# Kernel optimization log

Measured on AMD Instinct MI355X. Metric: run time of the kernel, lower is better.

Reference implementation:

```python
import jax, jax.numpy as jnp
import numpy as np

K = 10      # neighbors; conv width math 10 -> 3 -> 1
EPS = 1e-5  # InstanceNorm2d default eps (affine=False)
NEG = 0.2   # leaky relu slope


def _instnorm(x):
    m = x.mean(axis=(2, 3), keepdims=True)
    v = x.var(axis=(2, 3), keepdims=True)  # biased var, as in torch instance_norm
    return (x - m) * jax.lax.rsqrt(v + EPS)


def _conv13(x, w, b, s):
    y = jax.lax.conv_general_dilated(x, w, (1, s), 'VALID',
                                     dimension_numbers=('NCHW', 'OIHW', 'NCHW'))
    return y + b[None, :, None, None]


def _block(x, wA, bA, wB, bB):
    # Sequential(conv(1,3,stride(1,3)), IN, ReLU, conv(1,3), IN, ReLU)
    y = jax.nn.relu(_instnorm(_conv13(x, wA, bA, 3)))
    return jax.nn.relu(_instnorm(_conv13(y, wB, bB, 1)))


def _knn_idx(coords, k):
    # coords [B,2,N] -> k nearest neighbor indices [B,N,k] (self excluded)
    pts = coords.transpose(0, 2, 1)
    sq = (pts ** 2).sum(-1)
    dist = sq[:, :, None] + sq[:, None, :] - 2.0 * jnp.einsum('bnc,bmc->bnm', pts, pts)
    dist = jnp.clip(dist, 1e-12)
    _, idx = jax.lax.top_k(-dist, k + 1)  # smallest distances, sorted
    return idx[:, :, 1:]


def _gather_nb(x, idx):
    # x [B,C,N], idx [B,N,k] -> [B,C,N,k]
    return jax.vmap(lambda f, i: f[:, i])(x, idx)


def _graph_feat(feats, idx):
    nb = _gather_nb(feats, idx)
    ctr = jnp.broadcast_to(feats[..., None], nb.shape)
    return jnp.concatenate([ctr, nb - ctr], axis=1)  # [B,2C,N,k]


def _cos_angle(coords, idx):
    nei = _gather_nb(coords, idx)          # [B,2,N,k]
    ctr = coords[..., None]                # [B,2,N,1]
    dot = (ctr * nei).sum(axis=1, keepdims=True)
    na = jnp.sqrt((ctr ** 2).sum(axis=1, keepdims=True))
    nb = jnp.sqrt((nei ** 2).sum(axis=1, keepdims=True))
    return dot / (na * nb)                 # [B,1,N,k]


def _c1(w, x):
    # 1x1 conv, no bias
    return jnp.einsum('oi,bihw->bohw', w, x)


def _forward(coords, features, W1, W2, W3, W3o, a1wA, a1bA, a1wB, a1bB,
             a2wA, a2bA, a2wB, a2bB, angwA, angbA, angwB, angbB):
    B, C, N = features.shape
    lrelu = lambda x: jax.nn.leaky_relu(x, NEG)
    x0 = features[..., None]
    # KNN depends only on coords: all three torch graph builds give identical indices
    idx = _knn_idx(coords, K)
    x1_old = _graph_feat(features, idx)                         # [B,2C,N,K]
    x1 = _block(x1_old, a1wA, a1bA, a1wB, a1bB)                 # [B,C,N,1]
    # angle_enc1 is shared and idx identical -> f_ang1 == f_ang2
    f_ang = _block(_cos_angle(coords, idx), angwA, angbA, angwB, angbB)
    x2 = _block(_graph_feat(x1[..., 0], idx), a2wA, a2bA, a2wB, a2bB)
    x3 = jnp.concatenate([x0, x1 + f_ang, x2 + f_ang], axis=1)  # [B,3C,N,1]
    x3 = lrelu(_instnorm(_c1(W3, x3))).reshape(B, -1, N)
    x1o = lrelu(_instnorm(_c1(W1, x1_old))).max(axis=-1, keepdims=True)   # [B,C,N,1]
    x2o = lrelu(_instnorm(_c1(W2, _graph_feat(x1o[..., 0], idx)))).max(axis=-1, keepdims=True)
    x3o = jnp.concatenate([x0, x1o, x2o], axis=1)               # [B,4C,N,1]
    x3o = lrelu(_instnorm(_c1(W3o, x3o))).reshape(B, -1, N)
    return x3 + x3o


def setup_inputs():
    key = jax.random.key(0)
    ks = jax.random.split(key, 20)
    B, C, N = 4, 128, 4096
    r = lambda i, shp, sc=1.0: jax.random.normal(ks[i], shp, jnp.float32) * sc
    s = 0.05
    return {
        'coords': r(0, (B, 2, N)),
        'features': r(1, (B, C, N)),
        'W1': r(2, (C, 2 * C), s),
        'W2': r(3, (2 * C, 2 * C), s),
        'W3': r(4, (C, 3 * C), s),
        'W3o': r(5, (C, 4 * C), s),
        'a1wA': r(6, (C, 2 * C, 1, 3), s), 'a1bA': r(7, (C,), s),
        'a1wB': r(8, (C, C, 1, 3), s), 'a1bB': r(9, (C,), s),
        'a2wA': r(10, (C, 2 * C, 1, 3), s), 'a2bA': r(11, (C,), s),
        'a2wB': r(12, (C, C, 1, 3), s), 'a2bB': r(13, (C,), s),
        'angwA': r(14, (C, 1, 1, 3), s), 'angbA': r(15, (C,), s),
        'angwB': r(16, (C, C, 1, 3), s), 'angbB': r(17, (C,), s),
    }


def reference(coords, features, W1, W2, W3, W3o, a1wA, a1bA, a1wB, a1bB,
              a2wA, a2bA, a2wB, a2bB, angwA, angbA, angwB, angbB):
    return _forward(coords, features, W1, W2, W3, W3o, a1wA, a1bA, a1wB, a1bB,
                    a2wA, a2bA, a2wB, a2bB, angwA, angbA, angwB, angbB)
```

## Files before the change

kernel.cpp:

```cpp
#include <hip/hip_runtime.h>
#include <hip/hip_bf16.h>

typedef unsigned long long ull;

#define BN 4
#define CH 128
#define NP 4096
#define KNB 10
#define EPSI 1e-5f
#define GM_PTS 16
#define CA_PTS 16

#define FMA4(A, W, F) do { (A).x += (W).x*(F); (A).y += (W).y*(F); \
                           (A).z += (W).z*(F); (A).w += (W).w*(F); } while(0)

__device__ __forceinline__ ull shfl_xor_u64(ull v, int mask) {
    unsigned lo = (unsigned)(v & 0xFFFFFFFFu);
    unsigned hi = (unsigned)(v >> 32);
    lo = __shfl_xor(lo, mask);
    hi = __shfl_xor(hi, mask);
    return ((ull)hi << 32) | lo;
}

__device__ __forceinline__ int clampj(int j) { return ((unsigned)j < (unsigned)NP) ? j : 0; }

__device__ __forceinline__ unsigned short f2bf(float f) {
    unsigned u = __float_as_uint(f);
    unsigned r = u + 0x7FFFu + ((u >> 16) & 1u);
    return (unsigned short)(r >> 16);
}
__device__ __forceinline__ float bf2f(unsigned short h) {
    return __uint_as_float(((unsigned)h) << 16);
}
__device__ __forceinline__ float4 bfload4(const unsigned short* p) {
    ushort4 h = *(const ushort4*)p;
    float4 r; r.x = bf2f(h.x); r.y = bf2f(h.y); r.z = bf2f(h.z); r.w = bf2f(h.w);
    return r;
}
__device__ __forceinline__ ushort4 bf4(float4 x) {
    ushort4 h; h.x = f2bf(x.x); h.y = f2bf(x.y); h.z = f2bf(x.z); h.w = f2bf(x.w);
    return h;
}

__device__ __forceinline__ void d_packA(const float* w, float* WT, int i) {
    int co = i % CH, ci = (i / CH) % CH, s = i / (CH * CH);
    float val;
    if (s == 0) {
        val = 0.f;
        for (int dk = 0; dk < 3; dk++)
            val += w[(co * 256 + ci) * 3 + dk] - w[(co * 256 + 128 + ci) * 3 + dk];
    } else {
        val = w[(co * 256 + 128 + ci) * 3 + (s - 1)];
    }
    WT[i] = val;
}
__device__ __forceinline__ void d_packB(const float* w, float* WT, int i) {
    int co = i % CH, ci = (i / CH) % CH, dk = i / (CH * CH);
    WT[i] = w[(co * CH + ci) * 3 + dk];
}
__device__ __forceinline__ void d_packUV(const float* w, float* Wu, float* Wn, int Cout, int i) {
    int co = i % Cout, ci = i / Cout;
    float a = w[co * 256 + ci], bb = w[co * 256 + 128 + ci];
    Wu[i] = a - bb; Wn[i] = bb;
}
__device__ __forceinline__ void d_packP(const float* w, float* WT, int Cin, int Cout, int i) {
    int co = i % Cout, ci = i / Cout;
    WT[i] = w[co * Cin + ci];
}

__global__ void pack_all(const float* __restrict__ a1wA, const float* __restrict__ a2wA,
                         const float* __restrict__ a1wB, const float* __restrict__ a2wB,
                         const float* __restrict__ angwB, const float* __restrict__ W1,
                         const float* __restrict__ W2, const float* __restrict__ W3,
                         const float* __restrict__ W3o, const float* __restrict__ angwA,
                         float* __restrict__ WA1T, float* __restrict__ WA2T,
                         float* __restrict__ WB1T, float* __restrict__ WB2T,
                         float* __restrict__ WBAT,
                         float* __restrict__ W1U, float* __restrict__ W1N,
                         float* __restrict__ W2U, float* __restrict__ W2N,
                         float* __restrict__ W3T, float* __restrict__ W3OT,
                         float* __restrict__ WANGA) {
    int i = blockIdx.x * 256 + threadIdx.x;
    const int sA = 4 * CH * CH;
    const int sB = 3 * CH * CH;
    if (i < sA) { d_packA(a1wA, WA1T, i); return; } i -= sA;
    if (i < sA) { d_packA(a2wA, WA2T, i); return; } i -= sA;
    if (i < sB) { d_packB(a1wB, WB1T, i); return; } i -= sB;
    if (i < sB) { d_packB(a2wB, WB2T, i); return; } i -= sB;
    if (i < sB) { d_packB(angwB, WBAT, i); return; } i -= sB;
    if (i < CH * CH) { d_packUV(W1, W1U, W1N, CH, i); return; } i -= CH * CH;
    if (i < CH * 256) { d_packUV(W2, W2U, W2N, 256, i); return; } i -= CH * 256;
    if (i < 384 * CH) { d_packP(W3, W3T, 384, CH, i); return; } i -= 384 * CH;
    if (i < 512 * CH) { d_packP(W3o, W3OT, 512, CH, i); return; } i -= 512 * CH;
    if (i < 3 * CH) { d_packP(angwA, WANGA, 3, CH, i); return; }
}

__global__ void ftrans_kernel(const float* __restrict__ feats, float* __restrict__ F) {
    int i = blockIdx.x * 256 + threadIdx.x;
    if (i >= BN * CH * NP) return;
    int n = i % NP, c = (i / NP) % CH, b = i / (NP * CH);
    F[(b * NP + n) * CH + c] = feats[i];
}

__global__ void knn_kernel(const float* __restrict__ coords, int* __restrict__ IDX) {
    int gw = blockIdx.x * 4 + (threadIdx.x >> 6);
    int b = gw / NP;
    int n = gw % NP;
    int lane = threadIdx.x & 63;
    float xn = coords[(b * 2 + 0) * NP + n];
    float yn = coords[(b * 2 + 1) * NP + n];
    float sn = __fadd_rn(__fmul_rn(xn, xn), __fmul_rn(yn, yn));
    ull a[11];
    #pragma unroll
    for (int q = 0; q < 11; q++) a[q] = 0xFFFFFFFFFFFFFFFFULL;
    for (int m = lane; m < NP; m += 64) {
        float xm = coords[(b * 2 + 0) * NP + m];
        float ym = coords[(b * 2 + 1) * NP + m];
        float sm = __fadd_rn(__fmul_rn(xm, xm), __fmul_rn(ym, ym));
        float dot = __fmaf_rn(yn, ym, __fmul_rn(xn, xm));
        float d = __fsub_rn(__fadd_rn(sn, sm), __fmul_rn(2.0f, dot));
        d = fmaxf(d, 1e-12f);
        ull key = ((ull)__float_as_uint(d) << 32) | (unsigned)m;
        if (key < a[10]) {
            a[10] = key;
            #pragma unroll
            for (int q = 10; q > 0; --q)
                if (a[q] < a[q - 1]) { ull t = a[q]; a[q] = a[q - 1]; a[q - 1] = t; }
        }
    }
    for (int r = 0; r < 11; ++r) {
        ull k = a[0];
        ull mk = k;
        #pragma unroll
        for (int off = 1; off < 64; off <<= 1) {
            ull o = shfl_xor_u64(mk, off);
            mk = (o < mk) ? o : mk;
        }
        if (k == mk) {
            #pragma unroll
            for (int q = 0; q < 10; ++q) a[q] = a[q + 1];
            a[10] = 0xFFFFFFFFFFFFFFFFULL;
        }
        if (lane == 0 && r > 0) IDX[(b * NP + n) * KNB + (r - 1)] = (int)(mk & 0xFFFFFFFFu);
    }
}

__global__ void cosangle_kernel(const float* __restrict__ coords, const int* __restrict__ IDX,
                                float* __restrict__ COSA) {
    int i = blockIdx.x * 256 + threadIdx.x;
    if (i >= BN * NP * KNB) return;
    int n = (i / KNB) % NP, b = i / (KNB * NP);
    int j = clampj(IDX[i]);
    float xc = coords[(b * 2 + 0) * NP + n], yc = coords[(b * 2 + 1) * NP + n];
    float xm = coords[(b * 2 + 0) * NP + j], ym = coords[(b * 2 + 1) * NP + j];
    float dot = xc * xm + yc * ym;
    float na = sqrtf(xc * xc + yc * yc);
    float nb2 = sqrtf(xm * xm + ym * ym);
    COSA[i] = dot / fmaxf(na * nb2, 1e-30f);
}

__global__ __launch_bounds__(256) void convA_kernel(const float* __restrict__ Fin,
                             const int* __restrict__ IDX,
                             const float* __restrict__ WT, float* __restrict__ YA,
                             float* __restrict__ PART,
                             const float* __restrict__ STATS, int slot) {
    __shared__ __align__(16) float ctr[CA_PTS][CH];
    __shared__ __align__(16) unsigned short nbh[CA_PTS][9][CH];
    __shared__ int jidx[CA_PTS * 9];
    int b = blockIdx.x / (NP / CA_PTS);
    int chunk = blockIdx.x % (NP / CA_PTS);
    int n0 = chunk * CA_PTS;
    int cog = threadIdx.x & 31;
    int pg  = threadIdx.x >> 5;
    const float* SB = (slot >= 0) ? &STATS[((size_t)(slot * BN + b) * 256) * 2] : nullptr;
    if (threadIdx.x < CA_PTS * 9) {
        int n = threadIdx.x / 9, kk = threadIdx.x % 9;
        jidx[threadIdx.x] = clampj(IDX[(b * NP + n0 + n) * KNB + kk]);
    }
    __syncthreads();
    for (int v4 = threadIdx.x; v4 < CA_PTS * 32; v4 += 256) {
        int n = v4 >> 5, c4 = v4 & 31;
        float4 x = *(const float4*)&Fin[(size_t)(b * NP + n0 + n) * CH + c4 * 4];
        if (SB) {
            float4 s0 = *(const float4*)&SB[c4 * 8];
            float4 s1 = *(const float4*)&SB[c4 * 8 + 4];
            x.x = fmaxf((x.x - s0.x) * s0.y, 0.f);
            x.y = fmaxf((x.y - s0.z) * s0.w, 0.f);
            x.z = fmaxf((x.z - s1.x) * s1.y, 0.f);
            x.w = fmaxf((x.w - s1.z) * s1.w, 0.f);
        }
        *(float4*)&ctr[n][c4 * 4] = x;
    }
    for (int v4 = threadIdx.x; v4 < CA_PTS * 9 * 32; v4 += 256) {
        int n = v4 / 288, rem = v4 % 288, kk = rem >> 5, c4 = rem & 31;
        float4 x = *(const float4*)&Fin[(size_t)(b * NP + jidx[n * 9 + kk]) * CH + c4 * 4];
        if (SB) {
            float4 s0 = *(const float4*)&SB[c4 * 8];
            float4 s1 = *(const float4*)&SB[c4 * 8 + 4];
            x.x = fmaxf((x.x - s0.x) * s0.y, 0.f);
            x.y = fmaxf((x.y - s0.z) * s0.w, 0.f);
            x.z = fmaxf((x.z - s1.x) * s1.y, 0.f);
            x.w = fmaxf((x.w - s1.z) * s1.w, 0.f);
        }
        *(ushort4*)&nbh[n][kk][c4 * 4] = bf4(x);
    }
    __syncthreads();
    const float4* W4 = (const float4*)WT;
    const int p0 = pg * 2, p1 = pg * 2 + 1;
    float4 cacc0, cacc1;
    cacc0.x = cacc0.y = cacc0.z = cacc0.w = 0.f;
    cacc1 = cacc0;
    for (int ci = 0; ci < CH; ci += 4) {
        float4 xa = *(const float4*)&ctr[p0][ci];
        float4 xb = *(const float4*)&ctr[p1][ci];
        #pragma unroll
        for (int u = 0; u < 4; ++u) {
            float4 w = W4[(ci + u) * 32 + cog];
            float fa = ((const float*)&xa)[u];
            float fb = ((const float*)&xb)[u];
            FMA4(cacc0, w, fa); FMA4(cacc1, w, fb);
        }
    }
    float4 t00 = cacc0, t01 = cacc0, t02 = cacc0;
    float4 t10 = cacc1, t11 = cacc1, t12 = cacc1;
    for (int dk = 0; dk < 3; ++dk) {
        const float4* Wd = W4 + (size_t)(1 + dk) * (CH * 32);
        const unsigned short* a00 = &nbh[p0][0 * 3 + dk][0];
        const unsigned short* a01 = &nbh[p0][1 * 3 + dk][0];
        const unsigned short* a02 = &nbh[p0][2 * 3 + dk][0];
        const unsigned short* a10 = &nbh[p1][0 * 3 + dk][0];
        const unsigned short* a11 = &nbh[p1][1 * 3 + dk][0];
        const unsigned short* a12 = &nbh[p1][2 * 3 + dk][0];
        for (int ci = 0; ci < CH; ci += 4) {
            float4 x00 = bfload4(&a00[ci]);
            float4 x01 = bfload4(&a01[ci]);
            float4 x02 = bfload4(&a02[ci]);
            float4 x10 = bfload4(&a10[ci]);
            float4 x11 = bfload4(&a11[ci]);
            float4 x12 = bfload4(&a12[ci]);
            #pragma unroll
            for (int u = 0; u < 4; ++u) {
                float4 w = Wd[(ci + u) * 32 + cog];
                FMA4(t00, w, ((const float*)&x00)[u]);
                FMA4(t01, w, ((const float*)&x01)[u]);
                FMA4(t02, w, ((const float*)&x02)[u]);
                FMA4(t10, w, ((const float*)&x10)[u]);
                FMA4(t11, w, ((const float*)&x11)[u]);
                FMA4(t12, w, ((const float*)&x12)[u]);
            }
        }
    }
    {
        size_t base0 = ((size_t)(b * NP + n0 + p0) * 3) * CH + cog * 4;
        *(float4*)&YA[base0 + 0 * CH] = t00;
        *(float4*)&YA[base0 + 1 * CH] = t01;
        *(float4*)&YA[base0 + 2 * CH] = t02;
        size_t base1 = ((size_t)(b * NP + n0 + p1) * 3) * CH + cog * 4;
        *(float4*)&YA[base1 + 0 * CH] = t10;
        *(float4*)&YA[base1 + 1 * CH] = t11;
        *(float4*)&YA[base1 + 2 * CH] = t12;
    }
    float s4[4], q4[4];
    s4[0] = t00.x + t01.x + t02.x + t10.x + t11.x + t12.x;
    s4[1] = t00.y + t01.y + t02.y + t10.y + t11.y + t12.y;
    s4[2] = t00.z + t01.z + t02.z + t10.z + t11.z + t12.z;
    s4[3] = t00.w + t01.w + t02.w + t10.w + t11.w + t12.w;
    q4[0] = t00.x*t00.x + t01.x*t01.x + t02.x*t02.x + t10.x*t10.x + t11.x*t11.x + t12.x*t12.x;
    q4[1] = t00.y*t00.y + t01.y*t01.y + t02.y*t02.y + t10.y*t10.y + t11.y*t11.y + t12.y*t12.y;
    q4[2] = t00.z*t00.z + t01.z*t01.z + t02.z*t02.z + t10.z*t10.z + t11.z*t11.z + t12.z*t12.z;
    q4[3] = t00.w*t00.w + t01.w*t01.w + t02.w*t02.w + t10.w*t10.w + t11.w*t11.w + t12.w*t12.w;
    __syncthreads();
    float* red = (float*)&nbh[0][0][0];
    #pragma unroll
    for (int j = 0; j < 4; ++j) {
        red[((pg * 32 + cog) * 4 + j) * 2 + 0] = s4[j];
        red[((pg * 32 + cog) * 4 + j) * 2 + 1] = q4[j];
    }
    __syncthreads();
    if (threadIdx.x < CH) {
        int c = threadIdx.x;
        float ss = 0.f, qq = 0.f;
        #pragma unroll
        for (int g = 0; g < 8; ++g) {
            ss += red[((g * 32 + (c >> 2)) * 4 + (c & 3)) * 2 + 0];
            qq += red[((g * 32 + (c >> 2)) * 4 + (c & 3)) * 2 + 1];
        }
        PART[((size_t)(b * (NP / CA_PTS) + chunk) * 256 + c) * 2 + 0] = ss;
        PART[((size_t)(b * (NP / CA_PTS) + chunk) * 256 + c) * 2 + 1] = qq;
    }
}

__global__ void angA_kernel(const float* __restrict__ COSA, const float* __restrict__ WT,
                            float* __restrict__ YA, float* __restrict__ PART) {
    __shared__ float ca[32][10];
    int b = blockIdx.x / (NP / 32);
    int chunk = blockIdx.x % (NP / 32);
    int n0 = chunk * 32;
    int co = threadIdx.x;
    for (int v = threadIdx.x; v < 320; v += 128) {
        int nn = v / 10, kk = v % 10;
        ca[nn][kk] = COSA[(b * NP + n0 + nn) * KNB + kk];
    }
    float w0 = WT[co], w1 = WT[CH + co], w2 = WT[2 * CH + co];
    __syncthreads();
    float sum = 0.f, sq = 0.f;
    for (int nn = 0; nn < 32; nn++) {
        #pragma unroll
        for (int t = 0; t < 3; t++) {
            float v = w0 * ca[nn][3 * t] + w1 * ca[nn][3 * t + 1] + w2 * ca[nn][3 * t + 2];
            YA[((b * NP + n0 + nn) * 3 + t) * CH + co] = v;
            sum += v; sq += v * v;
        }
    }
    PART[((b * (NP / 32) + chunk) * 256 + co) * 2 + 0] = sum;
    PART[((b * (NP / 32) + chunk) * 256 + co) * 2 + 1] = sq;
}

template <int CIN, int NCOG>
__device__ __forceinline__ void gemm_16pt(const float* lds, const float* __restrict__ WT,
                                          int cog, int pg, float4 acc[4]) {
    const float4* W4 = (const float4*)WT;
    const float* xb = lds + pg * 4 * CIN;
    for (int ci = 0; ci < CIN; ci += 4) {
        float4 x0 = *(const float4*)&xb[0 * CIN + ci];
        float4 x1 = *(const float4*)&xb[1 * CIN + ci];
        float4 x2 = *(const float4*)&xb[2 * CIN + ci];
        float4 x3 = *(const float4*)&xb[3 * CIN + ci];
        #pragma unroll
        for (int u = 0; u < 4; ++u) {
            float4 w = W4[(ci + u) * NCOG + cog];
            float f0 = ((const float*)&x0)[u];
            float f1 = ((const float*)&x1)[u];
            float f2 = ((const float*)&x2)[u];
            float f3 = ((const float*)&x3)[u];
            FMA4(acc[0], w, f0); FMA4(acc[1], w, f1);
            FMA4(acc[2], w, f2); FMA4(acc[3], w, f3);
        }
    }
}

template <int NCOG>
__device__ __forceinline__ void reduce_stats(const float* s4, const float* q4,
                                             float* red, float* __restrict__ PART,
                                             int b, int chunk, int nchunks,
                                             int pg, int cog) {
    constexpr int COUT = NCOG * 4;
    __syncthreads();
    #pragma unroll
    for (int j = 0; j < 4; ++j) {
        red[((pg * NCOG + cog) * 4 + j) * 2 + 0] = s4[j];
        red[((pg * NCOG + cog) * 4 + j) * 2 + 1] = q4[j];
    }
    __syncthreads();
    int c = threadIdx.x;
    if (c < COUT) {
        float ss = 0.f, qq = 0.f;
        #pragma unroll
        for (int g = 0; g < 4; ++g) {
            ss += red[((g * NCOG + (c >> 2)) * 4 + (c & 3)) * 2 + 0];
            qq += red[((g * NCOG + (c >> 2)) * 4 + (c & 3)) * 2 + 1];
        }
        PART[((size_t)(b * nchunks + chunk) * 256 + c) * 2 + 0] = ss;
        PART[((size_t)(b * nchunks + chunk) * 256 + c) * 2 + 1] = qq;
    }
}

template <int NCOG>
__device__ __forceinline__ void out16(const float4 acc[4], float* __restrict__ OUT,
                                      int b, int n0, int pg, int cog,
                                      float s4[4], float q4[4]) {
    constexpr int COUT = NCOG * 4;
    #pragma unroll
    for (int p = 0; p < 4; ++p) {
        *(float4*)&OUT[(size_t)(b * NP + n0 + pg * 4 + p) * COUT + cog * 4] = acc[p];
        s4[0] += acc[p].x; s4[1] += acc[p].y; s4[2] += acc[p].z; s4[3] += acc[p].w;
        q4[0] += acc[p].x * acc[p].x; q4[1] += acc[p].y * acc[p].y;
        q4[2] += acc[p].z * acc[p].z; q4[3] += acc[p].w * acc[p].w;
    }
}

template <int CIN, int NCOG>
__global__ void pixel_gemm_t(const float* __restrict__ IN_, const float* __restrict__ WT,
                             float* __restrict__ OUT, const float* __restrict__ STATS,
                             int slot, int act, float* __restrict__ PART) {
    constexpr int COUT = NCOG * 4;
    constexpr int BD = 4 * NCOG;
    __shared__ __align__(16) float ldsin[16 * CIN];
    int b = blockIdx.x / (NP / 16);
    int chunk = blockIdx.x % (NP / 16);
    int n0 = chunk * 16;
    int cog = threadIdx.x & (NCOG - 1);
    int pg = threadIdx.x / NCOG;
    constexpr int nv4 = 16 * CIN / 4;
    if (slot >= 0) {
        int cbase = (4 * threadIdx.x) & 127;
        const float* st = &STATS[((slot * BN + b) * 256 + cbase) * 2];
        float m0 = st[0], r0 = st[1], m1 = st[2], r1 = st[3];
        float m2 = st[4], r2 = st[5], m3 = st[6], r3 = st[7];
        for (int v4 = threadIdx.x; v4 < nv4; v4 += BD) {
            float4 x = *(const float4*)&IN_[(size_t)(b * NP + n0) * CIN + 4 * v4];
            float v0 = (x.x - m0) * r0, v1 = (x.y - m1) * r1;
            float v2 = (x.z - m2) * r2, v3 = (x.w - m3) * r3;
            if (act) {
                x.x = (v0 >= 0.f) ? v0 : 0.2f * v0;
                x.y = (v1 >= 0.f) ? v1 : 0.2f * v1;
                x.z = (v2 >= 0.f) ? v2 : 0.2f * v2;
                x.w = (v3 >= 0.f) ? v3 : 0.2f * v3;
            } else {
                x.x = fmaxf(v0, 0.f); x.y = fmaxf(v1, 0.f);
                x.z = fmaxf(v2, 0.f); x.w = fmaxf(v3, 0.f);
            }
            *(float4*)&ldsin[4 * v4] = x;
        }
    } else {
        for (int v4 = threadIdx.x; v4 < nv4; v4 += BD)
            *(float4*)&ldsin[4 * v4] =
                *(const float4*)&IN_[(size_t)(b * NP + n0) * CIN + 4 * v4];
    }
    __syncthreads();
    float4 acc[4];
    #pragma unroll
    for (int p = 0; p < 4; ++p) acc[p].x = acc[p].y = acc[p].z = acc[p].w = 0.f;
    gemm_16pt<CIN, NCOG>(ldsin, WT, cog, pg, acc);
    float s4[4] = {0,0,0,0}, q4[4] = {0,0,0,0};
    out16<NCOG>(acc, OUT, b, n0, pg, cog, s4, q4);
    if (PART)
        reduce_stats<NCOG>(s4, q4, ldsin, PART, b, chunk, NP / 16, pg, cog);
}

__global__ void stats_final(const float* __restrict__ PART, float* __restrict__ STATS,
                            int S, int Cc, int slot, int nch) {
    __shared__ float ssum[256], ssq[256];
    int bc = blockIdx.x;
    int b = bc / Cc, c = bc % Cc;
    float sum = 0.f, sq = 0.f;
    for (int ch = threadIdx.x; ch < nch; ch += 256) {
        sum += PART[((b * nch + ch) * 256 + c) * 2 + 0];
        sq  += PART[((b * nch + ch) * 256 + c) * 2 + 1];
    }
    ssum[threadIdx.x] = sum; ssq[threadIdx.x] = sq;
    __syncthreads();
    for (int s = 128; s > 0; s >>= 1) {
        if (threadIdx.x < s) {
            ssum[threadIdx.x] += ssum[threadIdx.x + s];
            ssq[threadIdx.x]  += ssq[threadIdx.x + s];
        }
        __syncthreads();
    }
    if (threadIdx.x == 0) {
        float mean = ssum[0] / (float)S;
        float var = fmaxf(ssq[0] / (float)S - mean * mean, 0.f);
        STATS[((slot * BN + b) * 256 + c) * 2 + 0] = mean;
        STATS[((slot * BN + b) * 256 + c) * 2 + 1] = rsqrtf(var + EPSI);
    }
}

template <int NCOG>
__global__ void gathermax_t(const float* __restrict__ X, const float* __restrict__ Wu,
                            const float* __restrict__ V, const int* __restrict__ IDX,
                            float* __restrict__ M, float* __restrict__ PART,
                            const float* __restrict__ STATS, int slot) {
    constexpr int COUT = NCOG * 4;
    __shared__ __align__(16) float rows[GM_PTS * CH];
    int b = blockIdx.x / (NP / GM_PTS);
    int chunk = blockIdx.x % (NP / GM_PTS);
    int n0 = chunk * GM_PTS;
    int cog = threadIdx.x & (NCOG - 1);
    int pg = threadIdx.x / NCOG;
    if (slot >= 0) {
        int c0 = (4 * threadIdx.x) & 127;
        const float* st = &STATS[((slot * BN + b) * 256 + c0) * 2];
        float m0 = st[0], r0 = st[1], m1 = st[2], r1 = st[3];
        float m2 = st[4], r2 = st[5], m3 = st[6], r3 = st[7];
        for (int v4 = threadIdx.x; v4 < GM_PTS * CH / 4; v4 += COUT) {
            float4 x = *(const float4*)&X[(size_t)(b * NP + n0) * CH + v4 * 4];
            float v0 = (x.x - m0) * r0, v1 = (x.y - m1) * r1;
            float v2 = (x.z - m2) * r2, v3 = (x.w - m3) * r3;
            x.x = (v0 >= 0.f) ? v0 : 0.2f * v0;
            x.y = (v1 >= 0.f) ? v1 : 0.2f * v1;
            x.z = (v2 >= 0.f) ? v2 : 0.2f * v2;
            x.w = (v3 >= 0.f) ? v3 : 0.2f * v3;
            *(float4*)&rows[v4 * 4] = x;
        }
    } else {
        for (int v4 = threadIdx.x; v4 < GM_PTS * CH / 4; v4 += COUT)
            *(float4*)&rows[v4 * 4] = *(const float4*)&X[(size_t)(b * NP + n0) * CH + v4 * 4];
    }
    __syncthreads();
    float4 acc[4];
    #pragma unroll
    for (int p = 0; p < 4; ++p) acc[p].x = acc[p].y = acc[p].z = acc[p].w = 0.f;
    gemm_16pt<CH, NCOG>(rows, Wu, cog, pg, acc);
    float s4[4] = {0,0,0,0}, q4[4] = {0,0,0,0};
    #pragma unroll
    for (int p = 0; p < 4; ++p) {
        int nn = n0 + pg * 4 + p;
        float4 u = acc[p];
        float4 best; best.x = best.y = best.z = best.w = -3.4e38f;
        for (int k = 0; k < KNB; ++k) {
            int j = clampj(IDX[(b * NP + nn) * KNB + k]);
            float4 vv = *(const float4*)&V[(size_t)(b * NP + j) * COUT + cog * 4];
            vv.x += u.x; vv.y += u.y; vv.z += u.z; vv.w += u.w;
            s4[0] += vv.x; s4[1] += vv.y; s4[2] += vv.z; s4[3] += vv.w;
            q4[0] += vv.x * vv.x; q4[1] += vv.y * vv.y;
            q4[2] += vv.z * vv.z; q4[3] += vv.w * vv.w;
            best.x = fmaxf(best.x, vv.x); best.y = fmaxf(best.y, vv.y);
            best.z = fmaxf(best.z, vv.z); best.w = fmaxf(best.w, vv.w);
        }
        *(float4*)&M[(size_t)(b * NP + nn) * COUT + cog * 4] = best;
    }
    __syncthreads();
    reduce_stats<NCOG>(s4, q4, rows, PART, b, chunk, NP / GM_PTS, pg, cog);
}

__global__ void head3_kernel(const float* __restrict__ F, const float* __restrict__ X1,
                             const float* __restrict__ X2, const float* __restrict__ FANG,
                             const float* __restrict__ WT, float* __restrict__ Y3,
                             float* __restrict__ PART, const float* __restrict__ STATS) {
    __shared__ __align__(16) float lds[16 * 384];
    int b = blockIdx.x / (NP / 16);
    int chunk = blockIdx.x % (NP / 16);
    int n0 = chunk * 16;
    int cog = threadIdx.x & 31;
    int pg = threadIdx.x >> 5;
    const float* S1 = &STATS[((size_t)(1 * BN + b) * 256) * 2];
    const float* S5 = &STATS[((size_t)(5 * BN + b) * 256) * 2];
    const float* S3 = &STATS[((size_t)(3 * BN + b) * 256) * 2];
    for (int v4 = threadIdx.x; v4 < 16 * 96; v4 += 128) {
        int nn = v4 / 96, q4 = v4 % 96;
        int part = q4 >> 5, c4 = q4 & 31;
        size_t base = (size_t)(b * NP + n0 + nn) * CH + c4 * 4;
        float4 val;
        if (part == 0) val = *(const float4*)&F[base];
        else {
            const float* src = (part == 1) ? X1 : X2;
            const float* SX = (part == 1) ? S1 : S5;
            float4 xx = *(const float4*)&src[base];
            float4 aa = *(const float4*)&FANG[base];
            float4 sx0 = *(const float4*)&SX[c4 * 8];
            float4 sx1 = *(const float4*)&SX[c4 * 8 + 4];
            float4 sa0 = *(const float4*)&S3[c4 * 8];
            float4 sa1 = *(const float4*)&S3[c4 * 8 + 4];
            val.x = fmaxf((xx.x - sx0.x) * sx0.y, 0.f) + fmaxf((aa.x - sa0.x) * sa0.y, 0.f);
            val.y = fmaxf((xx.y - sx0.z) * sx0.w, 0.f) + fmaxf((aa.y - sa0.z) * sa0.w, 0.f);
            val.z = fmaxf((xx.z - sx1.x) * sx1.y, 0.f) + fmaxf((aa.z - sa1.x) * sa1.y, 0.f);
            val.w = fmaxf((xx.w - sx1.z) * sx1.w, 0.f) + fmaxf((aa.w - sa1.z) * sa1.w, 0.f);
        }
        *(float4*)&lds[v4 * 4] = val;
    }
    __syncthreads();
    float4 acc[4];
    #pragma unroll
    for (int p = 0; p < 4; ++p) acc[p].x = acc[p].y = acc[p].z = acc[p].w = 0.f;
    gemm_16pt<384, 32>(lds, WT, cog, pg, acc);
    float s4[4] = {0,0,0,0}, q4[4] = {0,0,0,0};
    out16<32>(acc, Y3, b, n0, pg, cog, s4, q4);
    reduce_stats<32>(s4, q4, lds, PART, b, chunk, NP / 16, pg, cog);
}

__global__ void head3o_kernel(const float* __restrict__ F, const float* __restrict__ X1O,
                              const float* __restrict__ X2O, const float* __restrict__ WT,
                              float* __restrict__ Y3O, float* __restrict__ PART,
                              const float* __restrict__ STATS) {
    __shared__ __align__(16) float lds[16 * 512];
    int b = blockIdx.x / (NP / 16);
    int chunk = blockIdx.x % (NP / 16);
    int n0 = chunk * 16;
    int cog = threadIdx.x & 31;
    int pg = threadIdx.x >> 5;
    const float* S6 = &STATS[((size_t)(6 * BN + b) * 256) * 2];
    const float* S7 = &STATS[((size_t)(7 * BN + b) * 256) * 2];
    for (int v4 = threadIdx.x; v4 < 16 * 128; v4 += 128) {
        int nn = v4 >> 7, q4 = v4 & 127;
        float4 val;
        if (q4 < 32) {
            val = *(const float4*)&F[(size_t)(b * NP + n0 + nn) * CH + q4 * 4];
        } else if (q4 < 64) {
            int c4 = q4 - 32;
            float4 x = *(const float4*)&X1O[(size_t)(b * NP + n0 + nn) * CH + c4 * 4];
            float4 s0 = *(const float4*)&S6[c4 * 8];
            float4 s1 = *(const float4*)&S6[c4 * 8 + 4];
            float v0 = (x.x - s0.x) * s0.y, v1 = (x.y - s0.z) * s0.w;
            float v2 = (x.z - s1.x) * s1.y, v3 = (x.w - s1.z) * s1.w;
            val.x = (v0 >= 0.f) ? v0 : 0.2f * v0;
            val.y = (v1 >= 0.f) ? v1 : 0.2f * v1;
            val.z = (v2 >= 0.f) ? v2 : 0.2f * v2;
            val.w = (v3 >= 0.f) ? v3 : 0.2f * v3;
        } else {
            int c4 = q4 - 64;
            float4 x = *(const float4*)&X2O[(size_t)(b * NP + n0 + nn) * 256 + c4 * 4];
            float4 s0 = *(const float4*)&S7[c4 * 8];
            float4 s1 = *(const float4*)&S7[c4 * 8 + 4];
            float v0 = (x.x - s0.x) * s0.y, v1 = (x.y - s0.z) * s0.w;
            float v2 = (x.z - s1.x) * s1.y, v3 = (x.w - s1.z) * s1.w;
            val.x = (v0 >= 0.f) ? v0 : 0.2f * v0;
            val.y = (v1 >= 0.f) ? v1 : 0.2f * v1;
            val.z = (v2 >= 0.f) ? v2 : 0.2f * v2;
            val.w = (v3 >= 0.f) ? v3 : 0.2f * v3;
        }
        *(float4*)&lds[v4 * 4] = val;
    }
    __syncthreads();
    float4 acc[4];
    #pragma unroll
    for (int p = 0; p < 4; ++p) acc[p].x = acc[p].y = acc[p].z = acc[p].w = 0.f;
    gemm_16pt<512, 32>(lds, WT, cog, pg, acc);
    float s4[4] = {0,0,0,0}, q4[4] = {0,0,0,0};
    out16<32>(acc, Y3O, b, n0, pg, cog, s4, q4);
    reduce_stats<32>(s4, q4, lds, PART, b, chunk, NP / 16, pg, cog);
}

__global__ void final_kernel(const float* __restrict__ Y3, const float* __restrict__ Y3O,
                             const float* __restrict__ STATS, float* __restrict__ out) {
    __shared__ float T[64][129];
    int b = blockIdx.x / (NP / 64);
    int n0 = (blockIdx.x % (NP / 64)) * 64;
    int co = threadIdx.x;
    float m3 = STATS[((8 * BN + b) * 256 + co) * 2 + 0];
    float r3 = STATS[((8 * BN + b) * 256 + co) * 2 + 1];
    float m3o = STATS[((9 * BN + b) * 256 + co) * 2 + 0];
    float r3o = STATS[((9 * BN + b) * 256 + co) * 2 + 1];
    for (int j = 0; j < 64; j++) {
        size_t idx = (size_t)(b * NP + n0 + j) * CH + co;
        float v3 = (Y3[idx] - m3) * r3;
        v3 = (v3 >= 0.f) ? v3 : 0.2f * v3;
        float v3o = (Y3O[idx] - m3o) * r3o;
        v3o = (v3o >= 0.f) ? v3o : 0.2f * v3o;
        T[j][co] = v3 + v3o;
    }
    __syncthreads();
    for (int rr = 0; rr < 64; rr++) {
        int r = rr * 2 + (threadIdx.x >> 6);
        int j = threadIdx.x & 63;
        out[(size_t)(b * CH + r) * NP + n0 + j] = T[j][r];
    }
}

extern "C" void kernel_launch(void* const* d_in, const int* in_sizes, int n_in,
                              void* d_out, int out_size, void* d_ws, size_t ws_size,
                              hipStream_t stream) {
    const float* coords   = (const float*)d_in[0];
    const float* features = (const float*)d_in[1];
    const float* W1   = (const float*)d_in[2];
    const float* W2   = (const float*)d_in[3];
    const float* W3   = (const float*)d_in[4];
    const float* W3o  = (const float*)d_in[5];
    const float* a1wA = (const float*)d_in[6];
    const float* a1wB = (const float*)d_in[8];
    const float* a2wA = (const float*)d_in[10];
    const float* a2wB = (const float*)d_in[12];
    const float* angwA = (const float*)d_in[14];
    const float* angwB = (const float*)d_in[16];
    float* out = (float*)d_out;
    float* ws = (float*)d_ws;
    (void)ws_size; (void)in_sizes; (void)n_in; (void)out_size;

    size_t off = 0;
    float* WA1T  = ws + off; off += 4 * CH * CH;
    float* WA2T  = ws + off; off += 4 * CH * CH;
    float* WB1T  = ws + off; off += 3 * CH * CH;
    float* WB2T  = ws + off; off += 3 * CH * CH;
    float* WBAT  = ws + off; off += 3 * CH * CH;
    float* WANGA = ws + off; off += 512;
    float* W1U   = ws + off; off += CH * CH;
    float* W1N   = ws + off; off += CH * CH;
    float* W2U   = ws + off; off += CH * 256;
    float* W2N   = ws + off; off += CH * 256;
    float* W3T   = ws + off; off += 384 * CH;
    float* W3OT  = ws + off; off += 512 * CH;
    int*   IDX   = (int*)(ws + off); off += (size_t)BN * NP * KNB;
    float* COSA  = ws + off; off += (size_t)BN * NP * KNB;
    float* PART  = ws + off; off += (size_t)BN * 1024 * 256 * 2;
    float* STATS = ws + off; off += 10 * BN * 256 * 2;
    const size_t UNIT = (size_t)BN * NP * CH;
    float* POOL  = ws + off; off += 7 * UNIT;

    float* F    = POOL + 0 * UNIT;
    float* YA   = POOL + 1 * UNIT;
    float* X1   = POOL + 4 * UNIT;
    float* FANG = POOL + 5 * UNIT;
    float* X2   = POOL + 6 * UNIT;
    float* Y3   = POOL + 1 * UNIT;
    float* V1   = POOL + 2 * UNIT;
    float* M1   = POOL + 6 * UNIT;
    float* V2   = POOL + 4 * UNIT;
    float* M2   = POOL + 2 * UNIT;
    float* Y3O  = POOL + 4 * UNIT;

    pack_all<<<1730, 256, 0, stream>>>(a1wA, a2wA, a1wB, a2wB, angwB, W1, W2, W3, W3o, angwA,
                                       WA1T, WA2T, WB1T, WB2T, WBAT,
                                       W1U, W1N, W2U, W2N, W3T, W3OT, WANGA);

    ftrans_kernel<<<(BN * CH * NP + 255) / 256, 256, 0, stream>>>(features, F);
    knn_kernel<<<BN * NP / 4, 256, 0, stream>>>(coords, IDX);
    cosangle_kernel<<<(BN * NP * KNB + 255) / 256, 256, 0, stream>>>(coords, IDX, COSA);

    auto sfin = [&](int S, int Cc, int slot, int nch) {
        stats_final<<<BN * Cc, 256, 0, stream>>>(PART, STATS, S, Cc, slot, nch);
    };

    convA_kernel<<<BN * (NP / CA_PTS), 256, 0, stream>>>(F, IDX, WA1T, YA, PART, STATS, -1);
    sfin(3 * NP, CH, 0, NP / CA_PTS);
    pixel_gemm_t<384, 32><<<BN * (NP / 16), 128, 0, stream>>>(YA, WB1T, X1, STATS, 0, 0, PART);
    sfin(NP, CH, 1, NP / 16);

    angA_kernel<<<BN * (NP / 32), 128, 0, stream>>>(COSA, WANGA, YA, PART);
    sfin(3 * NP, CH, 2, NP / 32);
    pixel_gemm_t<384, 32><<<BN * (NP / 16), 128, 0, stream>>>(YA, WBAT, FANG, STATS, 2, 0, PART);
    sfin(NP, CH, 3, NP / 16);

    convA_kernel<<<BN * (NP / CA_PTS), 256, 0, stream>>>(X1, IDX, WA2T, YA, PART, STATS, 1);
    sfin(3 * NP, CH, 4, NP / CA_PTS);
    pixel_gemm_t<384, 32><<<BN * (NP / 16), 128, 0, stream>>>(YA, WB2T, X2, STATS, 4, 0, PART);
    sfin(NP, CH, 5, NP / 16);

    head3_kernel<<<BN * (NP / 16), 128, 0, stream>>>(F, X1, X2, FANG, W3T, Y3, PART, STATS);
    sfin(NP, CH, 8, NP / 16);

    pixel_gemm_t<128, 32><<<BN * (NP / 16), 128, 0, stream>>>(F, W1N, V1, STATS, -1, 0, nullptr);
    gathermax_t<32><<<BN * (NP / GM_PTS), 128, 0, stream>>>(F, W1U, V1, IDX, M1, PART, STATS, -1);
    sfin(NP * KNB, CH, 6, NP / GM_PTS);

    pixel_gemm_t<128, 64><<<BN * (NP / 16), 256, 0, stream>>>(M1, W2N, V2, STATS, 6, 1, nullptr);
    gathermax_t<64><<<BN * (NP / GM_PTS), 256, 0, stream>>>(M1, W2U, V2, IDX, M2, PART, STATS, 6);
    sfin(NP * KNB, 256, 7, NP / GM_PTS);

    head3o_kernel<<<BN * (NP / 16), 128, 0, stream>>>(F, M1, M2, W3OT, Y3O, PART, STATS);
    sfin(NP, CH, 9, NP / 16);
    final_kernel<<<BN * (NP / 64), 128, 0, stream>>>(Y3, Y3O, STATS, out);
}
```

Measured before the change: 840.8 us.

## Fuse instance-norm stats finalization into producer kernels via atomics and last-block

```diff
diff --git a/kernel.cpp b/kernel.cpp
--- a/kernel.cpp
+++ b/kernel.cpp
@@ -40,6 +40,35 @@
 __device__ __forceinline__ ushort4 bf4(float4 x) {
     ushort4 h; h.x = f2bf(x.x); h.y = f2bf(x.y); h.z = f2bf(x.z); h.w = f2bf(x.w);
     return h;
+}
+
+__device__ __forceinline__ void stats_commit(float* __restrict__ SACC,
+                                             unsigned* __restrict__ CNT,
+                                             float* __restrict__ STATS,
+                                             int oslot, int b, int c, int valid,
+                                             float ss, float qq, int nblk, float Sdiv) {
+    __shared__ int isLast;
+    if (valid) {
+        atomicAdd(&SACC[((size_t)oslot * (BN * 256) + b * 256 + c) * 2 + 0], ss);
+        atomicAdd(&SACC[((size_t)oslot * (BN * 256) + b * 256 + c) * 2 + 1], qq);
+    }
+    __syncthreads();
+    if (threadIdx.x == 0) {
+        __threadfence();
+        unsigned old = atomicAdd(&CNT[oslot], 1u);
+        isLast = (old == (unsigned)(nblk - 1)) ? 1 : 0;
+    }
+    __syncthreads();
+    if (isLast) {
+        for (int i = threadIdx.x; i < BN * 256; i += blockDim.x) {
+            float sum = atomicAdd(&SACC[((size_t)oslot * (BN * 256) + i) * 2 + 0], 0.f);
+            float sq  = atomicAdd(&SACC[((size_t)oslot * (BN * 256) + i) * 2 + 1], 0.f);
+            float mean = sum / Sdiv;
+            float var = fmaxf(sq / Sdiv - mean * mean, 0.f);
+            STATS[((size_t)oslot * (BN * 256) + i) * 2 + 0] = mean;
+            STATS[((size_t)oslot * (BN * 256) + i) * 2 + 1] = rsqrtf(var + EPSI);
+        }
+    }
 }
 
 __device__ __forceinline__ void d_packA(const float* w, float* WT, int i) {
@@ -79,8 +108,12 @@
                          float* __restrict__ W1U, float* __restrict__ W1N,
                          float* __restrict__ W2U, float* __restrict__ W2N,
                          float* __restrict__ W3T, float* __restrict__ W3OT,
-                         float* __restrict__ WANGA) {
-    int i = blockIdx.x * 256 + threadIdx.x;
+                         float* __restrict__ WANGA,
+                         float* __restrict__ SACC, unsigned* __restrict__ CNT) {
+    int iz = blockIdx.x * 256 + threadIdx.x;
+    if (iz < 10 * BN * 256 * 2) SACC[iz] = 0.f;
+    if (iz < 10) CNT[iz] = 0u;
+    int i = iz;
     const int sA = 4 * CH * CH;
     const int sB = 3 * CH * CH;
     if (i < sA) { d_packA(a1wA, WA1T, i); return; } i -= sA;
@@ -162,8 +195,9 @@
 __global__ __launch_bounds__(256) void convA_kernel(const float* __restrict__ Fin,
                              const int* __restrict__ IDX,
                              const float* __restrict__ WT, float* __restrict__ YA,
-                             float* __restrict__ PART,
-                             const float* __restrict__ STATS, int slot) {
+                             const float* __restrict__ STATS_IN, int slot,
+                             float* __restrict__ SACC, unsigned* __restrict__ CNT,
+                             float* __restrict__ STATS, int oslot) {
     __shared__ __align__(16) float ctr[CA_PTS][CH];
     __shared__ __align__(16) unsigned short nbh[CA_PTS][9][CH];
     __shared__ int jidx[CA_PTS * 9];
@@ -172,7 +206,7 @@
     int n0 = chunk * CA_PTS;
     int cog = threadIdx.x & 31;
     int pg  = threadIdx.x >> 5;
-    const float* SB = (slot >= 0) ? &STATS[((size_t)(slot * BN + b) * 256) * 2] : nullptr;
+    const float* SB = (slot >= 0) ? &STATS_IN[((size_t)(slot * BN + b) * 256) * 2] : nullptr;
     if (threadIdx.x < CA_PTS * 9) {
         int n = threadIdx.x / 9, kk = threadIdx.x % 9;
         jidx[threadIdx.x] = clampj(IDX[(b * NP + n0 + n) * KNB + kk]);
@@ -277,21 +311,24 @@
         red[((pg * 32 + cog) * 4 + j) * 2 + 1] = q4[j];
     }
     __syncthreads();
-    if (threadIdx.x < CH) {
-        int c = threadIdx.x;
-        float ss = 0.f, qq = 0.f;
+    float ss = 0.f, qq = 0.f;
+    int c = threadIdx.x;
+    int valid = (c < CH);
+    if (valid) {
         #pragma unroll
         for (int g = 0; g < 8; ++g) {
             ss += red[((g * 32 + (c >> 2)) * 4 + (c & 3)) * 2 + 0];
             qq += red[((g * 32 + (c >> 2)) * 4 + (c & 3)) * 2 + 1];
         }
-        PART[((size_t)(b * (NP / CA_PTS) + chunk) * 256 + c) * 2 + 0] = ss;
-        PART[((size_t)(b * (NP / CA_PTS) + chunk) * 256 + c) * 2 + 1] = qq;
-    }
+    }
+    stats_commit(SACC, CNT, STATS, oslot, b, c, valid, ss, qq,
+                 BN * (NP / CA_PTS), 3.0f * NP);
 }
 
 __global__ void angA_kernel(const float* __restrict__ COSA, const float* __restrict__ WT,
-                            float* __restrict__ YA, float* __restrict__ PART) {
+                            float* __restrict__ YA,
+                            float* __restrict__ SACC, unsigned* __restrict__ CNT,
+                            float* __restrict__ STATS) {
     __shared__ float ca[32][10];
     int b = blockIdx.x / (NP / 32);
     int chunk = blockIdx.x % (NP / 32);
@@ -312,8 +349,7 @@
             sum += v; sq += v * v;
         }
     }
-    PART[((b * (NP / 32) + chunk) * 256 + co) * 2 + 0] = sum;
-    PART[((b * (NP / 32) + chunk) * 256 + co) * 2 + 1] = sq;
+    stats_commit(SACC, CNT, STATS, 2, b, co, 1, sum, sq, BN * (NP / 32), 3.0f * NP);
 }
 
 template <int CIN, int NCOG>
@@ -340,10 +376,13 @@
 }
 
 template <int NCOG>
-__device__ __forceinline__ void reduce_stats(const float* s4, const float* q4,
-                                             float* red, float* __restrict__ PART,
-                                             int b, int chunk, int nchunks,
-                                             int pg, int cog) {
+__device__ __forceinline__ void reduce_commit(const float* s4, const float* q4,
+                                              float* red,
+                                              float* __restrict__ SACC,
+                                              unsigned* __restrict__ CNT,
+                                              float* __restrict__ STATS,
+                                              int oslot, int b, int nblk, float Sdiv,
+                                              int pg, int cog) {
     constexpr int COUT = NCOG * 4;
     __syncthreads();
     #pragma unroll
@@ -353,16 +392,16 @@
     }
     __syncthreads();
     int c = threadIdx.x;
-    if (c < COUT) {
-        float ss = 0.f, qq = 0.f;
+    float ss = 0.f, qq = 0.f;
+    int valid = (c < COUT);
+    if (valid) {
         #pragma unroll
         for (int g = 0; g < 4; ++g) {
             ss += red[((g * NCOG + (c >> 2)) * 4 + (c & 3)) * 2 + 0];
             qq += red[((g * NCOG + (c >> 2)) * 4 + (c & 3)) * 2 + 1];
         }
-        PART[((size_t)(b * nchunks + chunk) * 256 + c) * 2 + 0] = ss;
-        PART[((size_t)(b * nchunks + chunk) * 256 + c) * 2 + 1] = qq;
-    }
+    }
+    stats_commit(SACC, CNT, STATS, oslot, b, c, valid, ss, qq, nblk, Sdiv);
 }
 
 template <int NCOG>
@@ -381,8 +420,10 @@
 
 template <int CIN, int NCOG>
 __global__ void pixel_gemm_t(const float* __restrict__ IN_, const float* __restrict__ WT,
-                             float* __restrict__ OUT, const float* __restrict__ STATS,
-                             int slot, int act, float* __restrict__ PART) {
+                             float* __restrict__ OUT, const float* __restrict__ STATS_IN,
+                             int slot, int act,
+                             float* __restrict__ SACC, unsigned* __restrict__ CNT,
+                             float* __restrict__ STATS, int oslot) {
     constexpr int COUT = NCOG * 4;
     constexpr int BD = 4 * NCOG;
     __shared__ __align__(16) float ldsin[16 * CIN];
@@ -394,7 +435,7 @@
     constexpr int nv4 = 16 * CIN / 4;
     if (slot >= 0) {
         int cbase = (4 * threadIdx.x) & 127;
-        const float* st = &STATS[((slot * BN + b) * 256 + cbase) * 2];
+        const float* st = &STATS_IN[((slot * BN + b) * 256 + cbase) * 2];
         float m0 = st[0], r0 = st[1], m1 = st[2], r1 = st[3];
         float m2 = st[4], r2 = st[5], m3 = st[6], r3 = st[7];
         for (int v4 = threadIdx.x; v4 < nv4; v4 += BD) {
@@ -424,42 +465,18 @@
     gemm_16pt<CIN, NCOG>(ldsin, WT, cog, pg, acc);
     float s4[4] = {0,0,0,0}, q4[4] = {0,0,0,0};
     out16<NCOG>(acc, OUT, b, n0, pg, cog, s4, q4);
-    if (PART)
-        reduce_stats<NCOG>(s4, q4, ldsin, PART, b, chunk, NP / 16, pg, cog);
-}
-
-__global__ void stats_final(const float* __restrict__ PART, float* __restrict__ STATS,
-                            int S, int Cc, int slot, int nch) {
-    __shared__ float ssum[256], ssq[256];
-    int bc = blockIdx.x;
-    int b = bc / Cc, c = bc % Cc;
-    float sum = 0.f, sq = 0.f;
-    for (int ch = threadIdx.x; ch < nch; ch += 256) {
-        sum += PART[((b * nch + ch) * 256 + c) * 2 + 0];
-        sq  += PART[((b * nch + ch) * 256 + c) * 2 + 1];
-    }
-    ssum[threadIdx.x] = sum; ssq[threadIdx.x] = sq;
-    __syncthreads();
-    for (int s = 128; s > 0; s >>= 1) {
-        if (threadIdx.x < s) {
-            ssum[threadIdx.x] += ssum[threadIdx.x + s];
-            ssq[threadIdx.x]  += ssq[threadIdx.x + s];
-        }
-        __syncthreads();
-    }
-    if (threadIdx.x == 0) {
-        float mean = ssum[0] / (float)S;
-        float var = fmaxf(ssq[0] / (float)S - mean * mean, 0.f);
-        STATS[((slot * BN + b) * 256 + c) * 2 + 0] = mean;
-        STATS[((slot * BN + b) * 256 + c) * 2 + 1] = rsqrtf(var + EPSI);
-    }
+    if (oslot >= 0)
+        reduce_commit<NCOG>(s4, q4, ldsin, SACC, CNT, STATS, oslot, b,
+                            BN * (NP / 16), (float)NP, pg, cog);
 }
 
 template <int NCOG>
 __global__ void gathermax_t(const float* __restrict__ X, const float* __restrict__ Wu,
                             const float* __restrict__ V, const int* __restrict__ IDX,
-                            float* __restrict__ M, float* __restrict__ PART,
-                            const float* __restrict__ STATS, int slot) {
+                            float* __restrict__ M, const float* __restrict__ STATS_IN,
+                            int slot,
+                            float* __restrict__ SACC, unsigned* __restrict__ CNT,
+                            float* __restrict__ STATS, int oslot) {
     constexpr int COUT = NCOG * 4;
     __shared__ __align__(16) float rows[GM_PTS * CH];
     int b = blockIdx.x / (NP / GM_PTS);
@@ -469,7 +486,7 @@
     int pg = threadIdx.x / NCOG;
     if (slot >= 0) {
         int c0 = (4 * threadIdx.x) & 127;
-        const float* st = &STATS[((slot * BN + b) * 256 + c0) * 2];
+        const float* st = &STATS_IN[((slot * BN + b) * 256 + c0) * 2];
         float m0 = st[0], r0 = st[1], m1 = st[2], r1 = st[3];
         float m2 = st[4], r2 = st[5], m3 = st[6], r3 = st[7];
         for (int v4 = threadIdx.x; v4 < GM_PTS * CH / 4; v4 += COUT) {
@@ -510,22 +527,25 @@
         *(float4*)&M[(size_t)(b * NP + nn) * COUT + cog * 4] = best;
     }
     __syncthreads();
-    reduce_stats<NCOG>(s4, q4, rows, PART, b, chunk, NP / GM_PTS, pg, cog);
+    reduce_commit<NCOG>(s4, q4, rows, SACC, CNT, STATS, oslot, b,
+                        BN * (NP / GM_PTS), (float)(NP * KNB), pg, cog);
 }
 
 __global__ void head3_kernel(const float* __restrict__ F, const float* __restrict__ X1,
                              const float* __restrict__ X2, const float* __restrict__ FANG,
                              const float* __restrict__ WT, float* __restrict__ Y3,
-                             float* __restrict__ PART, const float* __restrict__ STATS) {
+                             const float* __restrict__ STATS_IN,
+                             float* __restrict__ SACC, unsigned* __restrict__ CNT,
+                             float* __restrict__ STATS) {
     __shared__ __align__(16) float lds[16 * 384];
     int b = blockIdx.x / (NP / 16);
     int chunk = blockIdx.x % (NP / 16);
     int n0 = chunk * 16;
     int cog = threadIdx.x & 31;
     int pg = threadIdx.x >> 5;
-    const float* S1 = &STATS[((size_t)(1 * BN + b) * 256) * 2];
-    const float* S5 = &STATS[((size_t)(5 * BN + b) * 256) * 2];
-    const float* S3 = &STATS[((size_t)(3 * BN + b) * 256) * 2];
+    const float* S1 = &STATS_IN[((size_t)(1 * BN + b) * 256) * 2];
+    const float* S5 = &STATS_IN[((size_t)(5 * BN + b) * 256) * 2];
+    const float* S3 = &STATS_IN[((size_t)(3 * BN + b) * 256) * 2];
     for (int v4 = threadIdx.x; v4 < 16 * 96; v4 += 128) {
         int nn = v4 / 96, q4 = v4 % 96;
         int part = q4 >> 5, c4 = q4 & 31;
@@ -555,21 +575,23 @@
     gemm_16pt<384, 32>(lds, WT, cog, pg, acc);
     float s4[4] = {0,0,0,0}, q4[4] = {0,0,0,0};
     out16<32>(acc, Y3, b, n0, pg, cog, s4, q4);
-    reduce_stats<32>(s4, q4, lds, PART, b, chunk, NP / 16, pg, cog);
+    reduce_commit<32>(s4, q4, lds, SACC, CNT, STATS, 8, b,
+                      BN * (NP / 16), (float)NP, pg, cog);
 }
 
 __global__ void head3o_kernel(const float* __restrict__ F, const float* __restrict__ X1O,
                               const float* __restrict__ X2O, const float* __restrict__ WT,
-                              float* __restrict__ Y3O, float* __restrict__ PART,
-                              const float* __restrict__ STATS) {
+                              float* __restrict__ Y3O, const float* __restrict__ STATS_IN,
+                              float* __restrict__ SACC, unsigned* __restrict__ CNT,
+                              float* __restrict__ STATS) {
     __shared__ __align__(16) float lds[16 * 512];
     int b = blockIdx.x / (NP / 16);
     int chunk = blockIdx.x % (NP / 16);
     int n0 = chunk * 16;
     int cog = threadIdx.x & 31;
     int pg = threadIdx.x >> 5;
-    const float* S6 = &STATS[((size_t)(6 * BN + b) * 256) * 2];
-    const float* S7 = &STATS[((size_t)(7 * BN + b) * 256) * 2];
+    const float* S6 = &STATS_IN[((size_t)(6 * BN + b) * 256) * 2];
+    const float* S7 = &STATS_IN[((size_t)(7 * BN + b) * 256) * 2];
     for (int v4 = threadIdx.x; v4 < 16 * 128; v4 += 128) {
         int nn = v4 >> 7, q4 = v4 & 127;
         float4 val;
@@ -607,7 +629,8 @@
     gemm_16pt<512, 32>(lds, WT, cog, pg, acc);
     float s4[4] = {0,0,0,0}, q4[4] = {0,0,0,0};
     out16<32>(acc, Y3O, b, n0, pg, cog, s4, q4);
-    reduce_stats<32>(s4, q4, lds, PART, b, chunk, NP / 16, pg, cog);
+    reduce_commit<32>(s4, q4, lds, SACC, CNT, STATS, 9, b,
+                      BN * (NP / 16), (float)NP, pg, cog);
 }
 
 __global__ void final_kernel(const float* __restrict__ Y3, const float* __restrict__ Y3O,
@@ -687,45 +710,46 @@
     float* M2   = POOL + 2 * UNIT;
     float* Y3O  = POOL + 4 * UNIT;
 
+    float* SACC = PART + (1 << 20);
+    unsigned* CNT = (unsigned*)(SACC + 10 * BN * 256 * 2);
+
     pack_all<<<1730, 256, 0, stream>>>(a1wA, a2wA, a1wB, a2wB, angwB, W1, W2, W3, W3o, angwA,
                                        WA1T, WA2T, WB1T, WB2T, WBAT,
-                                       W1U, W1N, W2U, W2N, W3T, W3OT, WANGA);
+                                       W1U, W1N, W2U, W2N, W3T, W3OT, WANGA,
+                                       SACC, CNT);
 
     ftrans_kernel<<<(BN * CH * NP + 255) / 256, 256, 0, stream>>>(features, F);
     knn_kernel<<<BN * NP / 4, 256, 0, stream>>>(coords, IDX);
     cosangle_kernel<<<(BN * NP * KNB + 255) / 256, 256, 0, stream>>>(coords, IDX, COSA);
 
-    auto sfin = [&](int S, int Cc, int slot, int nch) {
-        stats_final<<<BN * Cc, 256, 0, stream>>>(PART, STATS, S, Cc, slot, nch);
-    };
-
-    convA_kernel<<<BN * (NP / CA_PTS), 256, 0, stream>>>(F, IDX, WA1T, YA, PART, STATS, -1);
-    sfin(3 * NP, CH, 0, NP / CA_PTS);
-    pixel_gemm_t<384, 32><<<BN * (NP / 16), 128, 0, stream>>>(YA, WB1T, X1, STATS, 0, 0, PART);
-    sfin(NP, CH, 1, NP / 16);
-
-    angA_kernel<<<BN * (NP / 32), 128, 0, stream>>>(COSA, WANGA, YA, PART);
-    sfin(3 * NP, CH, 2, NP / 32);
-    pixel_gemm_t<384, 32><<<BN * (NP / 16), 128, 0, stream>>>(YA, WBAT, FANG, STATS, 2, 0, PART);
-    sfin(NP, CH, 3, NP / 16);
-
-    convA_kernel<<<BN * (NP / CA_PTS), 256, 0, stream>>>(X1, IDX, WA2T, YA, PART, STATS, 1);
-    sfin(3 * NP, CH, 4, NP / CA_PTS);
-    pixel_gemm_t<384, 32><<<BN * (NP / 16), 128, 0, stream>>>(YA, WB2T, X2, STATS, 4, 0, PART);
-    sfin(NP, CH, 5, NP / 16);
-
-    head3_kernel<<<BN * (NP / 16), 128, 0, stream>>>(F, X1, X2, FANG, W3T, Y3, PART, STATS);
-    sfin(NP, CH, 8, NP / 16);
-
-    pixel_gemm_t<128, 32><<<BN * (NP / 16), 128, 0, stream>>>(F, W1N, V1, STATS, -1, 0, nullptr);
-    gathermax_t<32><<<BN * (NP / GM_PTS), 128, 0, stream>>>(F, W1U, V1, IDX, M1, PART, STATS, -1);
-    sfin(NP * KNB, CH, 6, NP / GM_PTS);
-
-    pixel_gemm_t<128, 64><<<BN * (NP / 16), 256, 0, stream>>>(M1, W2N, V2, STATS, 6, 1, nullptr);
-    gathermax_t<64><<<BN * (NP / GM_PTS), 256, 0, stream>>>(M1, W2U, V2, IDX, M2, PART, STATS, 6);
-    sfin(NP * KNB, 256, 7, NP / GM_PTS);
-
-    head3o_kernel<<<BN * (NP / 16), 128, 0, stream>>>(F, M1, M2, W3OT, Y3O, PART, STATS);
-    sfin(NP, CH, 9, NP / 16);
+    convA_kernel<<<BN * (NP / CA_PTS), 256, 0, stream>>>(F, IDX, WA1T, YA, STATS, -1,
+                                                         SACC, CNT, STATS, 0);
+    pixel_gemm_t<384, 32><<<BN * (NP / 16), 128, 0, stream>>>(YA, WB1T, X1, STATS, 0, 0,
+                                                              SACC, CNT, STATS, 1);
+
+    angA_kernel<<<BN * (NP / 32), 128, 0, stream>>>(COSA, WANGA, YA, SACC, CNT, STATS);
+    pixel_gemm_t<384, 32><<<BN * (NP / 16), 128, 0, stream>>>(YA, WBAT, FANG, STATS, 2, 0,
+                                                              SACC, CNT, STATS, 3);
+
+    convA_kernel<<<BN * (NP / CA_PTS), 256, 0, stream>>>(X1, IDX, WA2T, YA, STATS, 1,
+                                                         SACC, CNT, STATS, 4);
+    pixel_gemm_t<384, 32><<<BN * (NP / 16), 128, 0, stream>>>(YA, WB2T, X2, STATS, 4, 0,
+                                                              SACC, CNT, STATS, 5);
+
+    head3_kernel<<<BN * (NP / 16), 128, 0, stream>>>(F, X1, X2, FANG, W3T, Y3, STATS,
+                                                     SACC, CNT, STATS);
+
+    pixel_gemm_t<128, 32><<<BN * (NP / 16), 128, 0, stream>>>(F, W1N, V1, STATS, -1, 0,
+                                                              SACC, CNT, STATS, -1);
+    gathermax_t<32><<<BN * (NP / GM_PTS), 128, 0, stream>>>(F, W1U, V1, IDX, M1, STATS, -1,
+                                                            SACC, CNT, STATS, 6);
+
+    pixel_gemm_t<128, 64><<<BN * (NP / 16), 256, 0, stream>>>(M1, W2N, V2, STATS, 6, 1,
+                                                              SACC, CNT, STATS, -1);
+    gathermax_t<64><<<BN * (NP / GM_PTS), 256, 0, stream>>>(M1, W2U, V2, IDX, M2, STATS, 6,
+                                                            SACC, CNT, STATS, 7);
+
+    head3o_kernel<<<BN * (NP / 16), 128, 0, stream>>>(F, M1, M2, W3OT, Y3O, STATS,
+                                                      SACC, CNT, STATS);
     final_kernel<<<BN * (NP / 64), 128, 0, stream>>>(Y3, Y3O, STATS, out);
 }
```

New measurement: 1.145 ms. 36.2% more time.
